# Optimization experiments

Hardware: AMD Instinct MI355X
Metric: run time of the kernel (lower is better)

The kernel has to match this reference:

```python
import jax, jax.numpy as jnp
import numpy as np

# Llama-2-7B-like config with GQA
T, D, N, K, H = 2048, 4096, 32, 8, 128
THETA = 10000.0


def _rope(x, positions):
    """Split-ordering RoPE on last dim H of x: [..., T, heads, H]."""
    half = H // 2
    inv_freq = 1.0 / (THETA ** (jnp.arange(half, dtype=jnp.float32) / half))  # theta^(-2i/H)
    ang = positions.astype(jnp.float32)[:, None] * inv_freq[None, :]          # [T, half]
    cos = jnp.cos(ang)[:, None, :]
    sin = jnp.sin(ang)[:, None, :]
    x1, x2 = x[..., :half], x[..., half:]
    return jnp.concatenate([x1 * cos - x2 * sin, x2 * cos + x1 * sin], axis=-1).astype(x.dtype)


def setup_inputs() -> dict:
    key = jax.random.key(0)
    ks = jax.random.split(key, 5)
    s_in = 1.0 / np.sqrt(D)
    s_out = 1.0 / np.sqrt(N * H)
    return {
        "x": jax.random.normal(ks[0], (T, D), jnp.float32),
        "positions": jnp.arange(T, dtype=jnp.int32),
        "w_q": jax.random.normal(ks[1], (D, N, H), jnp.float32) * s_in,
        "w_k": jax.random.normal(ks[2], (D, K, H), jnp.float32) * s_in,
        "w_v": jax.random.normal(ks[3], (D, K, H), jnp.float32) * s_in,
        "w_o": jax.random.normal(ks[4], (N, H, D), jnp.float32) * s_out,
    }


def reference(x, positions, w_q, w_k, w_v, w_o):
    """Prefill path: fused QKV proj + RoPE + causal GQA attention + o_proj."""
    G = N // K  # query heads per kv head
    q = jnp.einsum('td,dnh->tnh', x, w_q)
    k = jnp.einsum('sd,dkh->skh', x, w_k)
    v = jnp.einsum('sd,dkh->skh', x, w_v)
    q = _rope(q, positions)
    k = _rope(k, positions)
    qg = q.reshape(T, K, G, H)
    scores = jnp.einsum('tkgh,skh->kgts', qg, k) * (H ** -0.5)
    causal = positions[:, None] >= positions[None, :]  # [T, S]
    scores = jnp.where(causal[None, None], scores, jnp.finfo(scores.dtype).min)
    probs = jax.nn.softmax(scores, axis=-1)
    out = jnp.einsum('kgts,skh->tkgh', probs, v).reshape(T, N, H)
    return jnp.einsum('tnh,nhd->td', out, w_o)
```

## Files before the change

kernel.cpp:

```cpp
#include <hip/hip_runtime.h>
#include <hip/hip_bf16.h>
#include <math.h>

#define T_SEQ   2048
#define D_MODEL 4096
#define N_Q     32
#define N_KV    8
#define HDIM    128
#define NH      (N_Q * HDIM)
#define KH      (N_KV * HDIM)
#define QKV_W   (NH + 2 * KH)

using bf16   = __hip_bfloat16;
using short8 = __attribute__((ext_vector_type(8))) short;
using floatx4 = __attribute__((ext_vector_type(4))) float;

__device__ __forceinline__ void load_lds16(const bf16* g, bf16* l) {
  __builtin_amdgcn_global_load_lds((const __attribute__((address_space(1))) void*)g,
                                   (__attribute__((address_space(3))) void*)l,
                                   16, 0, 0);
}

__global__ void cvt_bf16_kernel(const float* __restrict__ src, bf16* __restrict__ dst, int n4) {
  int i = blockIdx.x * 256 + threadIdx.x;
  if (i < n4) {
    const float4 v = ((const float4*)src)[i];
    union { bf16 h[4]; unsigned long long u; } o;
    o.h[0] = __float2bfloat16(v.x); o.h[1] = __float2bfloat16(v.y);
    o.h[2] = __float2bfloat16(v.z); o.h[3] = __float2bfloat16(v.w);
    ((unsigned long long*)dst)[i] = o.u;
  }
}

__global__ void sincos_tab(const int* __restrict__ pos, float* __restrict__ ct,
                           float* __restrict__ st) {
  const int i = blockIdx.x * 256 + threadIdx.x;
  const int t = i >> 6, h = i & 63;
  const float p = (float)pos[t];
  const float inv = exp2f(-(float)h * 0.20762050592420985f);
  float s, c; sincosf(p * inv, &s, &c);
  ct[i] = c; st[i] = s;
}

__global__ __launch_bounds__(256)
void transpose_cvt(const float* __restrict__ src, bf16* __restrict__ dst, int R, int C) {
  __shared__ float tile[64][65];
  const int bx = blockIdx.x * 64;
  const int by = blockIdx.y * 64;
  const int c4 = (threadIdx.x & 15) * 4;
  const int r0 = threadIdx.x >> 4;
#pragma unroll
  for (int i = 0; i < 4; i++) {
    const float4 v = *(const float4*)&src[(size_t)(by + r0 + i * 16) * C + bx + c4];
    tile[r0 + i * 16][c4 + 0] = v.x;
    tile[r0 + i * 16][c4 + 1] = v.y;
    tile[r0 + i * 16][c4 + 2] = v.z;
    tile[r0 + i * 16][c4 + 3] = v.w;
  }
  __syncthreads();
  const int cc = threadIdx.x >> 2;
  const int rq = (threadIdx.x & 3) * 16;
  union { bf16 h[8]; short8 s; } o0, o1;
#pragma unroll
  for (int j = 0; j < 8; j++) {
    o0.h[j] = __float2bfloat16(tile[rq + j][cc]);
    o1.h[j] = __float2bfloat16(tile[rq + 8 + j][cc]);
  }
  bf16* d = dst + (size_t)(bx + cc) * R + by + rq;
  *(short8*)(d)     = o0.s;
  *(short8*)(d + 8) = o1.s;
}

#define CS_STRIDE 137
template <int EPI>
__global__ __launch_bounds__(256)
void gemm_bt2(const bf16* __restrict__ A, const bf16* __restrict__ B,
              float* __restrict__ Cf, int N, int Kc,
              const float* __restrict__ cosT, const float* __restrict__ sinT,
              bf16* __restrict__ Qo, bf16* __restrict__ Ko, bf16* __restrict__ Vo) {
  __shared__ bf16 smem[(EPI == 2) ? (128 * CS_STRIDE) : (128 * 128)];
  bf16* As = smem;
  bf16* Bs = smem + 128 * 64;

  const int tid  = threadIdx.x;
  const int lane = tid & 63;
  const int wave = tid >> 6;
  const int bm = blockIdx.x * 128;
  const int bn = blockIdx.y * 128;
  const int wm = (wave >> 1) * 64;
  const int wn = (wave & 1) * 64;
  const int r = lane & 15, q = lane >> 4;

  floatx4 acc[4][4];
  const floatx4 zero = {0.f, 0.f, 0.f, 0.f};
#pragma unroll
  for (int i = 0; i < 4; i++)
#pragma unroll
    for (int j = 0; j < 4; j++) acc[i][j] = zero;

  const int rl = lane >> 3, ch = lane & 7;
  const int srow = wave * 32 + rl;
  const int gch = ch ^ rl;
  const bf16* gA = A + (size_t)(bm + srow) * Kc + gch * 8;
  const bf16* gB = B + (size_t)(bn + srow) * Kc + gch * 8;

  for (int k0 = 0; k0 < Kc; k0 += 64) {
    __syncthreads();
#pragma unroll
    for (int i = 0; i < 4; i++)
      load_lds16(gA + k0 + (size_t)i * 8 * Kc, As + (wave * 32 + i * 8) * 64);
#pragma unroll
    for (int i = 0; i < 4; i++)
      load_lds16(gB + k0 + (size_t)i * 8 * Kc, Bs + (wave * 32 + i * 8) * 64);
    __syncthreads();

#pragma unroll
    for (int ks = 0; ks < 2; ks++) {
      short8 af[4], bfr[4];
#pragma unroll
      for (int mt = 0; mt < 4; mt++)
        af[mt] = *(const short8*)(As + (wm + mt * 16 + r) * 64 + ((ks * 4 + q) ^ (r & 7)) * 8);
#pragma unroll
      for (int nt = 0; nt < 4; nt++)
        bfr[nt] = *(const short8*)(Bs + (wn + nt * 16 + r) * 64 + ((ks * 4 + q) ^ (r & 7)) * 8);
#pragma unroll
      for (int mt = 0; mt < 4; mt++)
#pragma unroll
        for (int nt = 0; nt < 4; nt++)
          acc[mt][nt] = __builtin_amdgcn_mfma_f32_16x16x32_bf16(af[mt], bfr[nt], acc[mt][nt], 0, 0, 0);
    }
  }

  if (EPI == 1) {
#pragma unroll
    for (int mt = 0; mt < 4; mt++)
#pragma unroll
      for (int nt = 0; nt < 4; nt++)
#pragma unroll
        for (int reg = 0; reg < 4; reg++) {
          const int row = bm + wm + mt * 16 + q * 4 + reg;
          const int col = bn + wn + nt * 16 + r;
          Cf[(size_t)row * N + col] = acc[mt][nt][reg];
        }
  } else {
    __syncthreads();
#pragma unroll
    for (int mt = 0; mt < 4; mt++)
#pragma unroll
      for (int nt = 0; nt < 4; nt++)
#pragma unroll
        for (int reg = 0; reg < 4; reg++)
          smem[(wm + mt * 16 + q * 4 + reg) * CS_STRIDE + wn + nt * 16 + r] =
              __float2bfloat16(acc[mt][nt][reg]);
    __syncthreads();

    const int hn = blockIdx.y;
    if (hn < N_Q + N_KV) {
      const float SCL = 0.12751744868673310f;
      const bool isQ = (hn < N_Q);
      bf16* base = isQ ? (Qo + (size_t)bm * NH + hn * HDIM)
                       : (Ko + (size_t)bm * KH + (hn - N_Q) * HDIM);
      const int ostride = isQ ? NH : KH;
      for (int idx = tid; idx < 128 * 64; idx += 256) {
        const int row = idx >> 6, h = idx & 63;
        const float x1 = __bfloat162float(smem[row * CS_STRIDE + h]);
        const float x2 = __bfloat162float(smem[row * CS_STRIDE + h + 64]);
        const float cs = cosT[(bm + row) * 64 + h];
        const float sn = sinT[(bm + row) * 64 + h];
        float o1 = x1 * cs - x2 * sn;
        float o2 = x2 * cs + x1 * sn;
        if (isQ) { o1 *= SCL; o2 *= SCL; }
        bf16* d = base + (size_t)row * ostride;
        d[h]      = __float2bfloat16(o1);
        d[h + 64] = __float2bfloat16(o2);
      }
    } else {
      const int kh = hn - (N_Q + N_KV);
      for (int idx = tid; idx < 128 * 32; idx += 256) {
        const int h = idx >> 5, r4 = (idx & 31) * 4;
        union { bf16 h4[4]; unsigned long long u; } o;
#pragma unroll
        for (int j = 0; j < 4; j++) o.h4[j] = smem[(r4 + j) * CS_STRIDE + h];
        *(unsigned long long*)(Vo + ((size_t)kh * HDIM + h) * T_SEQ + bm + r4) = o.u;
      }
    }
  }
}

#define MSHIFT 8.0f
__global__ __launch_bounds__(256, 2)
void flash_attn(const bf16* __restrict__ Q, const bf16* __restrict__ Kk,
                const bf16* __restrict__ Vt, bf16* __restrict__ O) {
  const int id = blockIdx.x;
  const int n  = id & 31;
  const int kh = n >> 2;
  const int bt = (id < 256) ? (15 - (id >> 5)) : ((id - 256) >> 5);
  const int t0 = bt * 128;
  const int tid = threadIdx.x, lane = tid & 63, w = tid >> 6;
  const int r = lane & 15, q = lane >> 4;

  __shared__ bf16 Ks[64][128];
  __shared__ bf16 Vs[128][64];
  __shared__ bf16 Ps[4][32][72];

  short8 qf[2][4];
#pragma unroll
  for (int mf = 0; mf < 2; mf++) {
    const bf16* qrow = Q + (size_t)(t0 + w * 32 + mf * 16 + r) * NH + n * HDIM;
#pragma unroll
    for (int ks = 0; ks < 4; ks++)
      qf[mf][ks] = *(const short8*)(qrow + ks * 32 + q * 8);
  }

  floatx4 o_acc[2][8];
  const floatx4 zero = {0.f, 0.f, 0.f, 0.f};
#pragma unroll
  for (int mf = 0; mf < 2; mf++)
#pragma unroll
    for (int i = 0; i < 8; i++) o_acc[mf][i] = zero;
  float l_lane[2][4];
#pragma unroll
  for (int mf = 0; mf < 2; mf++)
#pragma unroll
    for (int i = 0; i < 4; i++) l_lane[mf][i] = 0.f;

  const int krl = lane >> 4, kc = lane & 15;
  const int vrl = lane >> 3, vc = lane & 7;

  const int nIter = 2 * bt + 2;
  for (int it = 0; it < nIter; ++it) {
    const int s0 = it * 64;
    __syncthreads();
#pragma unroll
    for (int i = 0; i < 4; i++) {
      const int row = (w * 4 + i) * 4 + krl;
      load_lds16(Kk + (size_t)(s0 + row) * KH + kh * HDIM + (kc ^ (row & 7)) * 8,
                 &Ks[(w * 4 + i) * 4][0]);
    }
#pragma unroll
    for (int i = 0; i < 4; i++) {
      const int row = (w * 4 + i) * 8 + vrl;
      load_lds16(Vt + ((size_t)kh * HDIM + row) * T_SEQ + s0 + (vc ^ (row & 7)) * 8,
                 &Vs[(w * 4 + i) * 8][0]);
    }
    __syncthreads();

    floatx4 sa[2][4];
#pragma unroll
    for (int mf = 0; mf < 2; mf++)
#pragma unroll
      for (int nt = 0; nt < 4; nt++) sa[mf][nt] = zero;
#pragma unroll
    for (int ks = 0; ks < 4; ks++)
#pragma unroll
      for (int nt = 0; nt < 4; nt++) {
        const int krow = nt * 16 + r;
        const short8 kb = *(const short8*)(&Ks[krow][(((ks * 4 + q) ^ (krow & 7))) * 8]);
#pragma unroll
        for (int mf = 0; mf < 2; mf++)
          sa[mf][nt] = __builtin_amdgcn_mfma_f32_16x16x32_bf16(qf[mf][ks], kb, sa[mf][nt], 0, 0, 0);
      }

#pragma unroll
    for (int mf = 0; mf < 2; mf++) {
      const int rbase = t0 + w * 32 + mf * 16;
      if (s0 + 63 > rbase) {
#pragma unroll
        for (int nt = 0; nt < 4; nt++)
#pragma unroll
          for (int reg = 0; reg < 4; reg++) {
            const int trow = rbase + q * 4 + reg;
            const int scol = s0 + nt * 16 + r;
            if (scol > trow) sa[mf][nt][reg] = -INFINITY;
          }
      }
#pragma unroll
      for (int nt = 0; nt < 4; nt++)
#pragma unroll
        for (int reg = 0; reg < 4; reg++) {
          const float p = exp2f(sa[mf][nt][reg] - MSHIFT);
          l_lane[mf][reg] += p;
          Ps[w][mf * 16 + q * 4 + reg][nt * 16 + r] = __float2bfloat16(p);
        }
    }

    __asm__ volatile("s_waitcnt lgkmcnt(0)" ::: "memory");

#pragma unroll
    for (int ks = 0; ks < 2; ks++) {
      short8 pa[2];
#pragma unroll
      for (int mf = 0; mf < 2; mf++)
        pa[mf] = *(const short8*)(&Ps[w][mf * 16 + r][ks * 32 + q * 8]);
#pragma unroll
      for (int ht = 0; ht < 8; ht++) {
        const int vrow = ht * 16 + r;
        const short8 vb = *(const short8*)(&Vs[vrow][(((ks * 4 + q) ^ (vrow & 7))) * 8]);
#pragma unroll
        for (int mf = 0; mf < 2; mf++)
          o_acc[mf][ht] = __builtin_amdgcn_mfma_f32_16x16x32_bf16(pa[mf], vb, o_acc[mf][ht], 0, 0, 0);
      }
    }
  }

#pragma unroll
  for (int mf = 0; mf < 2; mf++)
#pragma unroll
    for (int reg = 0; reg < 4; reg++) {
      float v = l_lane[mf][reg];
      v += __shfl_xor(v, 1); v += __shfl_xor(v, 2);
      v += __shfl_xor(v, 4); v += __shfl_xor(v, 8);
      const float inv_l = 1.0f / v;
      const int trow = t0 + w * 32 + mf * 16 + q * 4 + reg;
#pragma unroll
      for (int ht = 0; ht < 8; ht++)
        O[(size_t)trow * NH + n * HDIM + ht * 16 + r] =
            __float2bfloat16(o_acc[mf][ht][reg] * inv_l);
    }
}

extern "C" void kernel_launch(void* const* d_in, const int* in_sizes, int n_in,
                              void* d_out, int out_size, void* d_ws, size_t ws_size,
                              hipStream_t stream) {
  (void)in_sizes; (void)n_in; (void)out_size; (void)ws_size;
  const float* x   = (const float*)d_in[0];
  const int* pos   = (const int*)d_in[1];
  const float* w_q = (const float*)d_in[2];
  const float* w_k = (const float*)d_in[3];
  const float* w_v = (const float*)d_in[4];
  const float* w_o = (const float*)d_in[5];
  float* out = (float*)d_out;

  char* ws = (char*)d_ws;
  bf16*  xb   = (bf16*)(ws);
  bf16*  Bq   = (bf16*)(ws + (16ULL << 20));
  bf16*  Qr   = (bf16*)(ws + (64ULL << 20));
  bf16*  Kr   = (bf16*)(ws + (80ULL << 20));
  bf16*  Vt   = (bf16*)(ws + (84ULL << 20));
  bf16*  Oatt = (bf16*)(ws + (88ULL << 20));
  float* ct   = (float*)(ws + (104ULL << 20));
  float* st   = (float*)(ws + (105ULL << 20));
  bf16*  woT  = Bq;

  cvt_bf16_kernel<<<(T_SEQ * D_MODEL / 4 + 255) / 256, 256, 0, stream>>>(x, xb, T_SEQ * D_MODEL / 4);
  sincos_tab<<<(T_SEQ * 64) / 256, 256, 0, stream>>>(pos, ct, st);
  transpose_cvt<<<dim3(NH / 64, D_MODEL / 64), 256, 0, stream>>>(w_q, Bq, D_MODEL, NH);
  transpose_cvt<<<dim3(KH / 64, D_MODEL / 64), 256, 0, stream>>>(w_k, Bq + (size_t)NH * D_MODEL, D_MODEL, KH);
  transpose_cvt<<<dim3(KH / 64, D_MODEL / 64), 256, 0, stream>>>(w_v, Bq + (size_t)(NH + KH) * D_MODEL, D_MODEL, KH);

  gemm_bt2<2><<<dim3(T_SEQ / 128, QKV_W / 128), 256, 0, stream>>>(
      xb, Bq, nullptr, QKV_W, D_MODEL, ct, st, Qr, Kr, Vt);

  transpose_cvt<<<dim3(D_MODEL / 64, NH / 64), 256, 0, stream>>>(w_o, woT, NH, D_MODEL);

  flash_attn<<<dim3(512), 256, 0, stream>>>(Qr, Kr, Vt, Oatt);

  gemm_bt2<1><<<dim3(T_SEQ / 128, D_MODEL / 128), 256, 0, stream>>>(
      Oatt, woT, out, D_MODEL, NH, nullptr, nullptr, nullptr, nullptr, nullptr);
}
```

Before: 490.8 us.

## Replace GEMM with 256x128-tile, 8-wave kernel using multi-stage async LDS pipeline

Replaces the single-buffered 128x128 GEMM with a 256x128 tile run by 512 threads. A is held in a three-slot LDS ring and B in a two-slot ring, with global-to-LDS loads issued ahead and interleaved between MFMA quadrants under explicit vmcnt waits, barriers and s_setprio. The goal is to hide global load latency behind MFMA work and to reuse each B tile across more rows. In exchange the LDS footprint and synchronisation get more complex, and there are fewer blocks, which can hurt occupancy or tail balance on the QKV and output projections.

```diff
diff --git a/kernel.cpp b/kernel.cpp
--- a/kernel.cpp
+++ b/kernel.cpp
@@ -71,25 +71,31 @@
   *(short8*)(d + 8) = o1.s;
 }
 
-#define CS_STRIDE 137
+#define A_SLOT 16384
+#define B_SLOT 8192
+#define B_BASE (3 * A_SLOT)
 template <int EPI>
-__global__ __launch_bounds__(256)
-void gemm_bt2(const bf16* __restrict__ A, const bf16* __restrict__ B,
-              float* __restrict__ Cf, int N, int Kc,
-              const float* __restrict__ cosT, const float* __restrict__ sinT,
-              bf16* __restrict__ Qo, bf16* __restrict__ Ko, bf16* __restrict__ Vo) {
-  __shared__ bf16 smem[(EPI == 2) ? (128 * CS_STRIDE) : (128 * 128)];
-  bf16* As = smem;
-  bf16* Bs = smem + 128 * 64;
-
+__global__ __launch_bounds__(512, 2)
+void gemm_p3(const bf16* __restrict__ A, const bf16* __restrict__ B,
+             float* __restrict__ Cf, int N, int Kc,
+             const float* __restrict__ cosT, const float* __restrict__ sinT,
+             bf16* __restrict__ Qo, bf16* __restrict__ Ko, bf16* __restrict__ Vo) {
+  __shared__ __align__(16) bf16 smem[3 * A_SLOT + 2 * B_SLOT];
   const int tid  = threadIdx.x;
   const int lane = tid & 63;
-  const int wave = tid >> 6;
-  const int bm = blockIdx.x * 128;
+  const int w    = tid >> 6;
+  const int bm = blockIdx.x * 256;
   const int bn = blockIdx.y * 128;
-  const int wm = (wave >> 1) * 64;
-  const int wn = (wave & 1) * 64;
+  const int wr = w >> 1;
+  const int wc = w & 1;
   const int r = lane & 15, q = lane >> 4;
+
+  const int rl = lane >> 3, ch = lane & 7;
+  const int swz = (ch ^ (rl & 7)) * 8;
+  const bf16* gA = A + (size_t)(bm + w * 32 + rl) * Kc + swz;
+  const bf16* gB = B + (size_t)(bn + w * 16 + rl) * Kc + swz;
+  const int ldsA0 = w * 32 * 64;
+  const int ldsB0 = w * 16 * 64;
 
   floatx4 acc[4][4];
   const floatx4 zero = {0.f, 0.f, 0.f, 0.f};
@@ -98,48 +104,90 @@
 #pragma unroll
     for (int j = 0; j < 4; j++) acc[i][j] = zero;
 
-  const int rl = lane >> 3, ch = lane & 7;
-  const int srow = wave * 32 + rl;
-  const int gch = ch ^ rl;
-  const bf16* gA = A + (size_t)(bm + srow) * Kc + gch * 8;
-  const bf16* gB = B + (size_t)(bn + srow) * Kc + gch * 8;
-
-  for (int k0 = 0; k0 < Kc; k0 += 64) {
-    __syncthreads();
+#pragma unroll
+  for (int t = 0; t < 2; t++) {
 #pragma unroll
     for (int i = 0; i < 4; i++)
-      load_lds16(gA + k0 + (size_t)i * 8 * Kc, As + (wave * 32 + i * 8) * 64);
-#pragma unroll
-    for (int i = 0; i < 4; i++)
-      load_lds16(gB + k0 + (size_t)i * 8 * Kc, Bs + (wave * 32 + i * 8) * 64);
-    __syncthreads();
-
-#pragma unroll
-    for (int ks = 0; ks < 2; ks++) {
-      short8 af[4], bfr[4];
-#pragma unroll
-      for (int mt = 0; mt < 4; mt++)
-        af[mt] = *(const short8*)(As + (wm + mt * 16 + r) * 64 + ((ks * 4 + q) ^ (r & 7)) * 8);
+      load_lds16(gA + t * 64 + (size_t)i * 8 * Kc, smem + t * A_SLOT + ldsA0 + i * 8 * 64);
+#pragma unroll
+    for (int j = 0; j < 2; j++)
+      load_lds16(gB + t * 64 + (size_t)j * 8 * Kc, smem + B_BASE + t * B_SLOT + ldsB0 + j * 8 * 64);
+  }
+
+#define RD_A(H)                                                                 \
+  _Pragma("unroll") for (int m2 = 0; m2 < 2; m2++)                              \
+  _Pragma("unroll") for (int ks = 0; ks < 2; ks++)                              \
+    aT[H][m2][ks] = *(const short8*)(As + (wr * 64 + (H) * 32 + m2 * 16 + r) * 64 \
+                                        + (((ks * 4 + q) ^ (r & 7)) * 8));
+#define RD_B(H)                                                                 \
+  _Pragma("unroll") for (int n2 = 0; n2 < 2; n2++)                              \
+  _Pragma("unroll") for (int ks = 0; ks < 2; ks++)                              \
+    bT[H][n2][ks] = *(const short8*)(Bs + (wc * 64 + (H) * 32 + n2 * 16 + r) * 64 \
+                                        + (((ks * 4 + q) ^ (r & 7)) * 8));
+#define MM(MQ, NQ)                                                              \
+  __builtin_amdgcn_s_setprio(1);                                                \
+  _Pragma("unroll") for (int ks = 0; ks < 2; ks++)                              \
+  _Pragma("unroll") for (int m2 = 0; m2 < 2; m2++)                              \
+  _Pragma("unroll") for (int n2 = 0; n2 < 2; n2++)                              \
+    acc[(MQ)*2+m2][(NQ)*2+n2] = __builtin_amdgcn_mfma_f32_16x16x32_bf16(        \
+        aT[MQ][m2][ks], bT[NQ][n2][ks], acc[(MQ)*2+m2][(NQ)*2+n2], 0, 0, 0);    \
+  __builtin_amdgcn_s_setprio(0);
+#define ST_A(i) load_lds16(gA + kA + (size_t)(i) * 8 * Kc, SdA + (i) * 8 * 64)
+#define ST_B(j) load_lds16(gB + kB + (size_t)(j) * 8 * Kc, SdB + (j) * 8 * 64)
+
+  const int NT = Kc >> 6;
+  int a_ring = 0;
+  for (int g = 0; g < NT; ++g) {
+    if (g == 0)          asm volatile("s_waitcnt vmcnt(6)" ::: "memory");
+    else if (g + 1 < NT) asm volatile("s_waitcnt vmcnt(4)" ::: "memory");
+    else                 asm volatile("s_waitcnt vmcnt(0)" ::: "memory");
+    __builtin_amdgcn_s_barrier();
+
+    const bf16* As = smem + a_ring * A_SLOT;
+    const bf16* Bs = smem + B_BASE + (g & 1) * B_SLOT;
+    int sa = a_ring - 1; if (sa < 0) sa = 2;
+    bf16* SdA = smem + sa * A_SLOT + ldsA0;
+    bf16* SdB = smem + B_BASE + ((g + 1) & 1) * B_SLOT + ldsB0;
+    const bool stA = (g + 2 < NT);
+    const bool stB = (g >= 1) && (g + 1 < NT);
+    const int kA = (g + 2) * 64, kB = (g + 1) * 64;
+
+    short8 aT[2][2][2], bT[2][2][2];
+    RD_A(0); RD_B(0);
+    if (stB) { ST_B(0); ST_B(1); }
+    __builtin_amdgcn_s_barrier();
+    MM(0, 0);
+    __builtin_amdgcn_s_barrier();
+    RD_B(1);
+    if (stA) { ST_A(0); ST_A(1); }
+    __builtin_amdgcn_s_barrier();
+    MM(0, 1);
+    __builtin_amdgcn_s_barrier();
+    RD_A(1);
+    if (stA) { ST_A(2); }
+    __builtin_amdgcn_s_barrier();
+    MM(1, 1);
+    __builtin_amdgcn_s_barrier();
+    if (stA) { ST_A(3); }
+    MM(1, 0);
+
+    a_ring = (a_ring + 1 == 3) ? 0 : a_ring + 1;
+  }
+#undef RD_A
+#undef RD_B
+#undef MM
+#undef ST_A
+#undef ST_B
+
+  if (EPI == 1) {
+#pragma unroll
+    for (int mt = 0; mt < 4; mt++)
 #pragma unroll
       for (int nt = 0; nt < 4; nt++)
-        bfr[nt] = *(const short8*)(Bs + (wn + nt * 16 + r) * 64 + ((ks * 4 + q) ^ (r & 7)) * 8);
-#pragma unroll
-      for (int mt = 0; mt < 4; mt++)
-#pragma unroll
-        for (int nt = 0; nt < 4; nt++)
-          acc[mt][nt] = __builtin_amdgcn_mfma_f32_16x16x32_bf16(af[mt], bfr[nt], acc[mt][nt], 0, 0, 0);
-    }
-  }
-
-  if (EPI == 1) {
-#pragma unroll
-    for (int mt = 0; mt < 4; mt++)
-#pragma unroll
-      for (int nt = 0; nt < 4; nt++)
 #pragma unroll
         for (int reg = 0; reg < 4; reg++) {
-          const int row = bm + wm + mt * 16 + q * 4 + reg;
-          const int col = bn + wn + nt * 16 + r;
+          const int row = bm + wr * 64 + mt * 16 + q * 4 + reg;
+          const int col = bn + wc * 64 + nt * 16 + r;
           Cf[(size_t)row * N + col] = acc[mt][nt][reg];
         }
   } else {
@@ -150,7 +198,7 @@
       for (int nt = 0; nt < 4; nt++)
 #pragma unroll
         for (int reg = 0; reg < 4; reg++)
-          smem[(wm + mt * 16 + q * 4 + reg) * CS_STRIDE + wn + nt * 16 + r] =
+          smem[(wr * 64 + mt * 16 + q * 4 + reg) * 137 + wc * 64 + nt * 16 + r] =
               __float2bfloat16(acc[mt][nt][reg]);
     __syncthreads();
 
@@ -161,10 +209,10 @@
       bf16* base = isQ ? (Qo + (size_t)bm * NH + hn * HDIM)
                        : (Ko + (size_t)bm * KH + (hn - N_Q) * HDIM);
       const int ostride = isQ ? NH : KH;
-      for (int idx = tid; idx < 128 * 64; idx += 256) {
+      for (int idx = tid; idx < 256 * 64; idx += 512) {
         const int row = idx >> 6, h = idx & 63;
-        const float x1 = __bfloat162float(smem[row * CS_STRIDE + h]);
-        const float x2 = __bfloat162float(smem[row * CS_STRIDE + h + 64]);
+        const float x1 = __bfloat162float(smem[row * 137 + h]);
+        const float x2 = __bfloat162float(smem[row * 137 + h + 64]);
         const float cs = cosT[(bm + row) * 64 + h];
         const float sn = sinT[(bm + row) * 64 + h];
         float o1 = x1 * cs - x2 * sn;
@@ -176,11 +224,11 @@
       }
     } else {
       const int kh = hn - (N_Q + N_KV);
-      for (int idx = tid; idx < 128 * 32; idx += 256) {
-        const int h = idx >> 5, r4 = (idx & 31) * 4;
+      for (int idx = tid; idx < 128 * 64; idx += 512) {
+        const int h = idx >> 6, r4 = (idx & 63) * 4;
         union { bf16 h4[4]; unsigned long long u; } o;
 #pragma unroll
-        for (int j = 0; j < 4; j++) o.h4[j] = smem[(r4 + j) * CS_STRIDE + h];
+        for (int j = 0; j < 4; j++) o.h4[j] = smem[(r4 + j) * 137 + h];
         *(unsigned long long*)(Vo + ((size_t)kh * HDIM + h) * T_SEQ + bm + r4) = o.u;
       }
     }
@@ -348,13 +396,13 @@
   transpose_cvt<<<dim3(KH / 64, D_MODEL / 64), 256, 0, stream>>>(w_k, Bq + (size_t)NH * D_MODEL, D_MODEL, KH);
   transpose_cvt<<<dim3(KH / 64, D_MODEL / 64), 256, 0, stream>>>(w_v, Bq + (size_t)(NH + KH) * D_MODEL, D_MODEL, KH);
 
-  gemm_bt2<2><<<dim3(T_SEQ / 128, QKV_W / 128), 256, 0, stream>>>(
+  gemm_p3<2><<<dim3(T_SEQ / 256, QKV_W / 128), 512, 0, stream>>>(
       xb, Bq, nullptr, QKV_W, D_MODEL, ct, st, Qr, Kr, Vt);
 
   transpose_cvt<<<dim3(D_MODEL / 64, NH / 64), 256, 0, stream>>>(w_o, woT, NH, D_MODEL);
 
   flash_attn<<<dim3(512), 256, 0, stream>>>(Qr, Kr, Vt, Oatt);
 
-  gemm_bt2<1><<<dim3(T_SEQ / 128, D_MODEL / 128), 256, 0, stream>>>(
+  gemm_p3<1><<<dim3(T_SEQ / 256, D_MODEL / 128), 512, 0, stream>>>(
       Oatt, woT, out, D_MODEL, NH, nullptr, nullptr, nullptr, nullptr, nullptr);
 }
```

Measured after the change: 510.0 us. 3.9% more time.
